# Kernel tuning notes

Measured on AMD Instinct MI355X. Metric: run time of the kernel, lower is better.

Reference implementation:

```python
import jax, jax.numpy as jnp
import numpy as np

B = 16
PATCH_NUM = 32      # L of inter branch
PATCH_SIZE = 128    # L of intra branch
WIN_SIZE = PATCH_NUM * PATCH_SIZE  # 4096
H = 8
E = 64


def setup_inputs() -> dict:
    key = jax.random.key(0)
    ks = jax.random.split(key, 6)
    return {
        "q_inter": jax.random.normal(ks[0], (B, PATCH_NUM, H, E), jnp.float32),
        "k_inter": jax.random.normal(ks[1], (B, PATCH_NUM, H, E), jnp.float32),
        "v_inter": jax.random.normal(ks[2], (B, PATCH_NUM, H, E), jnp.float32),
        "q_intra": jax.random.normal(ks[3], (B, PATCH_SIZE, H, E), jnp.float32),
        "k_intra": jax.random.normal(ks[4], (B, PATCH_SIZE, H, E), jnp.float32),
        "v_intra": jax.random.normal(ks[5], (B, PATCH_SIZE, H, E), jnp.float32),
    }


def _full_attention(q, k, v):
    # q,k,v: [B, L, H, E]; full softmax attention, scale = 1/sqrt(E)
    scale = 1.0 / jnp.sqrt(jnp.asarray(q.shape[-1], q.dtype))
    score = jnp.einsum('blhe,bshe->bhls', q, k) * scale
    att = jax.nn.softmax(score, axis=-1)  # dropout is identity in eval mode
    return jnp.einsum('bhls,bshd->blhd', att, v)


def reference(q_inter, k_inter, v_inter, q_intra, k_intra, v_intra):
    V_inter = _full_attention(q_inter, k_inter, v_inter)  # [B, patch_num, H, E]
    V_intra = _full_attention(q_intra, k_intra, v_intra)  # [B, patch_size, H, E]
    # einops repeat 'b pn h d -> b (pn ps) h d': each patch repeated ps times
    V_inter_up = jnp.repeat(V_inter, PATCH_SIZE, axis=1)  # [B, win_size, H, E]
    # einops repeat 'b ps h d -> b (ps pn) h d': each position repeated pn times
    V_intra_up = jnp.repeat(V_intra, PATCH_NUM, axis=1)   # [B, win_size, H, E]
    return V_inter_up + V_intra_up
```

## Files before the change

kernel.cpp:

```cpp
#include <hip/hip_runtime.h>


#define NH 8
#define NE 64
#define ROWSTRIDE (NH * NE)

__device__ __forceinline__ float dot4(const float4 a, const float4 b) {
    return a.x * b.x + a.y * b.y + a.z * b.z + a.w * b.w;
}

template <int L>
__global__ __launch_bounds__(256) void attn_kernel(
    const float* __restrict__ qg_, const float* __restrict__ kg_,
    const float* __restrict__ vg_, float* __restrict__ dst)
{
    constexpr int TILES = L / 32;
    constexpr int CPT   = L / 32;
    constexpr int SST   = L + 1;
    constexpr int KST   = 68;
    constexpr int QST   = 68;
    constexpr int VST   = 64;

    __shared__ __align__(16) float Ks[L * KST];
    __shared__ __align__(16) float Vs[L * VST];
    __shared__ __align__(16) float Qs[32 * QST];
    __shared__ float S[32 * SST];

    const int tid  = threadIdx.x;
    const int bid  = blockIdx.x;
    const int tile = bid % TILES;
    const int h    = (bid / TILES) % NH;
    const int b    = bid / (TILES * NH);
    const int r0   = tile * 32;

    const float* kg = kg_ + ((size_t)b * L * NH + h) * NE;
    const float* vg = vg_ + ((size_t)b * L * NH + h) * NE;
    const float* qg = qg_ + ((size_t)(b * L + r0) * NH + h) * NE;

    for (int idx = tid; idx < L * 16; idx += 256) {
        const int row = idx >> 4;
        const int f   = (idx & 15) * 4;
        *(float4*)&Ks[row * KST + f] = *(const float4*)(kg + (size_t)row * ROWSTRIDE + f);
        *(float4*)&Vs[row * VST + f] = *(const float4*)(vg + (size_t)row * ROWSTRIDE + f);
    }
    for (int idx = tid; idx < 32 * 16; idx += 256) {
        const int row = idx >> 4;
        const int f   = (idx & 15) * 4;
        *(float4*)&Qs[row * QST + f] = *(const float4*)(qg + (size_t)row * ROWSTRIDE + f);
    }
    __syncthreads();

    {
        const int rg = tid >> 5;
        const int cg = tid & 31;
        const int rr = rg * 4;
        float acc[4][CPT];
        #pragma unroll
        for (int i = 0; i < 4; i++)
            #pragma unroll
            for (int j = 0; j < CPT; j++) acc[i][j] = 0.f;

        #pragma unroll
        for (int e = 0; e < NE; e += 4) {
            float4 qv[4], kv[CPT];
            #pragma unroll
            for (int i = 0; i < 4; i++) qv[i] = *(const float4*)&Qs[(rr + i) * QST + e];
            #pragma unroll
            for (int j = 0; j < CPT; j++) kv[j] = *(const float4*)&Ks[(cg + j * 32) * KST + e];
            #pragma unroll
            for (int i = 0; i < 4; i++)
                #pragma unroll
                for (int j = 0; j < CPT; j++)
                    acc[i][j] += dot4(qv[i], kv[j]);
        }
        #pragma unroll
        for (int i = 0; i < 4; i++)
            #pragma unroll
            for (int j = 0; j < CPT; j++)
                S[(rr + i) * SST + cg + j * 32] = acc[i][j] * 0.125f;
    }
    __syncthreads();

    const int r   = tid >> 3;
    const int sub = tid & 7;
    float m = -1e30f;
    for (int c = 0; c < L; c++) m = fmaxf(m, S[r * SST + c]);
    float sum = 0.f;
    for (int c = 0; c < L; c++) sum += __expf(S[r * SST + c] - m);
    const float inv = 1.f / sum;
    __syncthreads();
    for (int c = sub; c < L; c += 8)
        S[r * SST + c] = __expf(S[r * SST + c] - m);
    __syncthreads();

    const int e0 = sub * 8;
    float a0=0,a1=0,a2=0,a3=0,a4=0,a5=0,a6=0,a7=0;
    for (int c = 0; c < L; c++) {
        const float p  = S[r * SST + c];
        const float4 va = *(const float4*)&Vs[c * VST + e0];
        const float4 vb = *(const float4*)&Vs[c * VST + e0 + 4];
        a0 += p * va.x; a1 += p * va.y; a2 += p * va.z; a3 += p * va.w;
        a4 += p * vb.x; a5 += p * vb.y; a6 += p * vb.z; a7 += p * vb.w;
    }
    const float4 oA = make_float4(a0 * inv, a1 * inv, a2 * inv, a3 * inv);
    const float4 oB = make_float4(a4 * inv, a5 * inv, a6 * inv, a7 * inv);

    float* w = dst + ((size_t)(b * L + r0 + r) * NH + h) * NE + e0;
    *(float4*)w       = oA;
    *(float4*)(w + 4) = oB;
}

__global__ __launch_bounds__(256) void upsample_add_kernel(
    const float4* __restrict__ wsI, const float4* __restrict__ wsT,
    float4* __restrict__ out)
{
    const int t  = blockIdx.x * 256 + threadIdx.x;
    const int e4 = t & 15;
    const int h  = (t >> 4) & 7;
    const int g  = (t >> 7) & 3;
    const int pn = (t >> 9) & 31;
    const int b  = t >> 14;

    const float4 a = wsI[((b * 32 + pn) * NH + h) * 16 + e4];
    const float4 c = wsT[((b * 128 + pn * 4 + g) * NH + h) * 16 + e4];
    const float4 s = make_float4(a.x + c.x, a.y + c.y, a.z + c.z, a.w + c.w);

    float4* o = out + ((((size_t)b * 4096 + pn * 128 + g * 32) * NH + h) * 16 + e4);
    #pragma unroll
    for (int j = 0; j < 32; j++)
        o[(size_t)j * (ROWSTRIDE / 4)] = s;
}

extern "C" void kernel_launch(void* const* d_in, const int* in_sizes, int n_in,
                              void* d_out, int out_size, void* d_ws, size_t ws_size,
                              hipStream_t stream) {
    const float* q_inter = (const float*)d_in[0];
    const float* k_inter = (const float*)d_in[1];
    const float* v_inter = (const float*)d_in[2];
    const float* q_intra = (const float*)d_in[3];
    const float* k_intra = (const float*)d_in[4];
    const float* v_intra = (const float*)d_in[5];
    float* out = (float*)d_out;
    float* wsI = (float*)d_ws;
    float* wsT = wsI + (size_t)16 * 32 * NH * NE;

    attn_kernel<32><<<16 * 8, 256, 0, stream>>>(q_inter, k_inter, v_inter, wsI);

    attn_kernel<128><<<16 * 8 * 4, 256, 0, stream>>>(q_intra, k_intra, v_intra, wsT);

    upsample_add_kernel<<<1024, 256, 0, stream>>>(
        (const float4*)wsI, (const float4*)wsT, (float4*)out);
}
```

Measured before the change: 191.2 us.

## Fuse both attention branches into one launch with register softmax and nontemporal stores

Merges the inter and intra attention kernels into a single launch that interleaves the two block types and shares one shared-memory buffer. The score buffer now reuses the K region. Softmax is computed from registers with warp shuffles instead of serial per-row loops over shared memory, and P·V reads probabilities as float4. The upsample kernel switches to nontemporal stores. The aim is to cut launch overhead, the serial softmax cost and cache pollution from the large output write, at the cost of a larger fixed shared footprint for the small blocks.

```diff
diff --git a/kernel.cpp b/kernel.cpp
--- a/kernel.cpp
+++ b/kernel.cpp
@@ -5,29 +5,26 @@
 #define NE 64
 #define ROWSTRIDE (NH * NE)
 
+typedef float vf4 __attribute__((ext_vector_type(4)));
+
 __device__ __forceinline__ float dot4(const float4 a, const float4 b) {
     return a.x * b.x + a.y * b.y + a.z * b.z + a.w * b.w;
 }
 
 template <int L>
-__global__ __launch_bounds__(256) void attn_kernel(
-    const float* __restrict__ qg_, const float* __restrict__ kg_,
-    const float* __restrict__ vg_, float* __restrict__ dst)
+__device__ __forceinline__ void attn_block(
+    const int bid, const float* __restrict__ qg_, const float* __restrict__ kg_,
+    const float* __restrict__ vg_, float* __restrict__ dst,
+    float* sKs, float* sVs, float* sQs)
 {
     constexpr int TILES = L / 32;
     constexpr int CPT   = L / 32;
-    constexpr int SST   = L + 1;
+    constexpr int SST   = L + 4;
     constexpr int KST   = 68;
     constexpr int QST   = 68;
     constexpr int VST   = 64;
 
-    __shared__ __align__(16) float Ks[L * KST];
-    __shared__ __align__(16) float Vs[L * VST];
-    __shared__ __align__(16) float Qs[32 * QST];
-    __shared__ float S[32 * SST];
-
     const int tid  = threadIdx.x;
-    const int bid  = blockIdx.x;
     const int tile = bid % TILES;
     const int h    = (bid / TILES) % NH;
     const int b    = bid / (TILES * NH);
@@ -40,79 +37,103 @@
     for (int idx = tid; idx < L * 16; idx += 256) {
         const int row = idx >> 4;
         const int f   = (idx & 15) * 4;
-        *(float4*)&Ks[row * KST + f] = *(const float4*)(kg + (size_t)row * ROWSTRIDE + f);
-        *(float4*)&Vs[row * VST + f] = *(const float4*)(vg + (size_t)row * ROWSTRIDE + f);
+        *(float4*)&sKs[row * KST + f] = *(const float4*)(kg + (size_t)row * ROWSTRIDE + f);
+        *(float4*)&sVs[row * VST + f] = *(const float4*)(vg + (size_t)row * ROWSTRIDE + f);
     }
     for (int idx = tid; idx < 32 * 16; idx += 256) {
         const int row = idx >> 4;
         const int f   = (idx & 15) * 4;
-        *(float4*)&Qs[row * QST + f] = *(const float4*)(qg + (size_t)row * ROWSTRIDE + f);
+        *(float4*)&sQs[row * QST + f] = *(const float4*)(qg + (size_t)row * ROWSTRIDE + f);
     }
     __syncthreads();
 
-    {
-        const int rg = tid >> 5;
-        const int cg = tid & 31;
-        const int rr = rg * 4;
-        float acc[4][CPT];
+    const int rg = tid >> 5;
+    const int cg = tid & 31;
+    const int rr = rg * 4;
+    float acc[4][CPT];
+    #pragma unroll
+    for (int i = 0; i < 4; i++)
         #pragma unroll
-        for (int i = 0; i < 4; i++)
-            #pragma unroll
-            for (int j = 0; j < CPT; j++) acc[i][j] = 0.f;
+        for (int j = 0; j < CPT; j++) acc[i][j] = 0.f;
 
+    #pragma unroll
+    for (int e = 0; e < NE; e += 4) {
+        float4 qv[4], kv[CPT];
         #pragma unroll
-        for (int e = 0; e < NE; e += 4) {
-            float4 qv[4], kv[CPT];
-            #pragma unroll
-            for (int i = 0; i < 4; i++) qv[i] = *(const float4*)&Qs[(rr + i) * QST + e];
-            #pragma unroll
-            for (int j = 0; j < CPT; j++) kv[j] = *(const float4*)&Ks[(cg + j * 32) * KST + e];
-            #pragma unroll
-            for (int i = 0; i < 4; i++)
-                #pragma unroll
-                for (int j = 0; j < CPT; j++)
-                    acc[i][j] += dot4(qv[i], kv[j]);
-        }
+        for (int i = 0; i < 4; i++) qv[i] = *(const float4*)&sQs[(rr + i) * QST + e];
+        #pragma unroll
+        for (int j = 0; j < CPT; j++) kv[j] = *(const float4*)&sKs[(cg + j * 32) * KST + e];
         #pragma unroll
         for (int i = 0; i < 4; i++)
             #pragma unroll
             for (int j = 0; j < CPT; j++)
-                S[(rr + i) * SST + cg + j * 32] = acc[i][j] * 0.125f;
+                acc[i][j] += dot4(qv[i], kv[j]);
+    }
+    __syncthreads();
+
+    float* S = sKs;
+
+    #pragma unroll
+    for (int i = 0; i < 4; i++) {
+        float m = acc[i][0] * 0.125f;
+        #pragma unroll
+        for (int j = 1; j < CPT; j++) m = fmaxf(m, acc[i][j] * 0.125f);
+        #pragma unroll
+        for (int msk = 1; msk < 32; msk <<= 1) m = fmaxf(m, __shfl_xor(m, msk));
+        float p[CPT], s = 0.f;
+        #pragma unroll
+        for (int j = 0; j < CPT; j++) { p[j] = __expf(acc[i][j] * 0.125f - m); s += p[j]; }
+        #pragma unroll
+        for (int msk = 1; msk < 32; msk <<= 1) s += __shfl_xor(s, msk);
+        const float inv = 1.f / s;
+        #pragma unroll
+        for (int j = 0; j < CPT; j++)
+            S[(rr + i) * SST + cg + 32 * j] = p[j] * inv;
     }
     __syncthreads();
 
     const int r   = tid >> 3;
     const int sub = tid & 7;
-    float m = -1e30f;
-    for (int c = 0; c < L; c++) m = fmaxf(m, S[r * SST + c]);
-    float sum = 0.f;
-    for (int c = 0; c < L; c++) sum += __expf(S[r * SST + c] - m);
-    const float inv = 1.f / sum;
-    __syncthreads();
-    for (int c = sub; c < L; c += 8)
-        S[r * SST + c] = __expf(S[r * SST + c] - m);
-    __syncthreads();
+    const int e0  = sub * 8;
+    float a0=0,a1=0,a2=0,a3=0,a4=0,a5=0,a6=0,a7=0;
+    for (int c0 = 0; c0 < L; c0 += 4) {
+        const float4 p4 = *(const float4*)&S[r * SST + c0];
+        const float pv[4] = { p4.x, p4.y, p4.z, p4.w };
+        #pragma unroll
+        for (int u = 0; u < 4; u++) {
+            const float p  = pv[u];
+            const float4 va = *(const float4*)&sVs[(c0 + u) * VST + e0];
+            const float4 vb = *(const float4*)&sVs[(c0 + u) * VST + e0 + 4];
+            a0 += p * va.x; a1 += p * va.y; a2 += p * va.z; a3 += p * va.w;
+            a4 += p * vb.x; a5 += p * vb.y; a6 += p * vb.z; a7 += p * vb.w;
+        }
+    }
+    float* w = dst + ((size_t)(b * L + r0 + r) * NH + h) * NE + e0;
+    *(float4*)w       = make_float4(a0, a1, a2, a3);
+    *(float4*)(w + 4) = make_float4(a4, a5, a6, a7);
+}
 
-    const int e0 = sub * 8;
-    float a0=0,a1=0,a2=0,a3=0,a4=0,a5=0,a6=0,a7=0;
-    for (int c = 0; c < L; c++) {
-        const float p  = S[r * SST + c];
-        const float4 va = *(const float4*)&Vs[c * VST + e0];
-        const float4 vb = *(const float4*)&Vs[c * VST + e0 + 4];
-        a0 += p * va.x; a1 += p * va.y; a2 += p * va.z; a3 += p * va.w;
-        a4 += p * vb.x; a5 += p * vb.y; a6 += p * vb.z; a7 += p * vb.w;
-    }
-    const float4 oA = make_float4(a0 * inv, a1 * inv, a2 * inv, a3 * inv);
-    const float4 oB = make_float4(a4 * inv, a5 * inv, a6 * inv, a7 * inv);
+__global__ __launch_bounds__(256, 2) void attn_fused(
+    const float* __restrict__ qI, const float* __restrict__ kI, const float* __restrict__ vI,
+    const float* __restrict__ qT, const float* __restrict__ kT, const float* __restrict__ vT,
+    float* __restrict__ wsI, float* __restrict__ wsT)
+{
+    __shared__ __align__(16) float sKs[128 * 68];
+    __shared__ __align__(16) float sVs[128 * 64];
+    __shared__ __align__(16) float sQs[32 * 68];
 
-    float* w = dst + ((size_t)(b * L + r0 + r) * NH + h) * NE + e0;
-    *(float4*)w       = oA;
-    *(float4*)(w + 4) = oB;
+    const int bid = blockIdx.x;
+    const int grp = bid / 5;
+    const int rem = bid - grp * 5;
+    if (rem < 4)
+        attn_block<128>(grp * 4 + rem, qT, kT, vT, wsT, sKs, sVs, sQs);
+    else
+        attn_block<32>(grp, qI, kI, vI, wsI, sKs, sVs, sQs);
 }
 
 __global__ __launch_bounds__(256) void upsample_add_kernel(
     const float4* __restrict__ wsI, const float4* __restrict__ wsT,
-    float4* __restrict__ out)
+    float* __restrict__ out)
 {
     const int t  = blockIdx.x * 256 + threadIdx.x;
     const int e4 = t & 15;
@@ -123,12 +144,13 @@
 
     const float4 a = wsI[((b * 32 + pn) * NH + h) * 16 + e4];
     const float4 c = wsT[((b * 128 + pn * 4 + g) * NH + h) * 16 + e4];
-    const float4 s = make_float4(a.x + c.x, a.y + c.y, a.z + c.z, a.w + c.w);
+    vf4 s;
+    s.x = a.x + c.x; s.y = a.y + c.y; s.z = a.z + c.z; s.w = a.w + c.w;
 
-    float4* o = out + ((((size_t)b * 4096 + pn * 128 + g * 32) * NH + h) * 16 + e4);
+    float* o = out + ((((size_t)b * 4096 + pn * 128 + g * 32) * NH + h) * 16 + e4) * 4;
     #pragma unroll
     for (int j = 0; j < 32; j++)
-        o[(size_t)j * (ROWSTRIDE / 4)] = s;
+        __builtin_nontemporal_store(s, (vf4*)(o + (size_t)j * ROWSTRIDE));
 }
 
 extern "C" void kernel_launch(void* const* d_in, const int* in_sizes, int n_in,
@@ -144,10 +166,9 @@
     float* wsI = (float*)d_ws;
     float* wsT = wsI + (size_t)16 * 32 * NH * NE;
 
-    attn_kernel<32><<<16 * 8, 256, 0, stream>>>(q_inter, k_inter, v_inter, wsI);
-
-    attn_kernel<128><<<16 * 8 * 4, 256, 0, stream>>>(q_intra, k_intra, v_intra, wsT);
+    attn_fused<<<640, 256, 0, stream>>>(
+        q_inter, k_inter, v_inter, q_intra, k_intra, v_intra, wsI, wsT);
 
     upsample_add_kernel<<<1024, 256, 0, stream>>>(
-        (const float4*)wsI, (const float4*)wsT, (float4*)out);
+        (const float4*)wsI, (const float4*)wsT, out);
 }
```

Measured after the change: 184.0 us. -3.8%, faster.
